# Optimization experiments

Measured on AMD Instinct MI355X. Metric: run time of the kernel, lower is better.

The kernel has to match this reference:

```python
import jax, jax.numpy as jnp
import numpy as np

NEG_INF = -1e30


def setup_inputs() -> dict:
    key = jax.random.key(0)
    k1, k2, k3, k4 = jax.random.split(key, 4)
    B, T, C, H = 4, 4096, 1024, 64
    x = jax.random.normal(k1, (B, T, C), dtype=jnp.float32)
    Wk = jax.random.normal(k2, (C, H), dtype=jnp.float32) * (C ** -0.5)
    Wq = jax.random.normal(k3, (C, H), dtype=jnp.float32) * (C ** -0.5)
    Wv = jax.random.normal(k4, (C, H), dtype=jnp.float32) * (C ** -0.5)
    return {"x": x, "Wk": Wk, "Wq": Wq, "Wv": Wv}


def reference(x, Wk, Wq, Wv):
    # x: [B, T, C]; Wq/Wk/Wv: [C, H]
    B, T, C = x.shape
    q = jnp.einsum('btc,ch->bth', x, Wq)  # [B,T,H]
    k = jnp.einsum('btc,ch->bth', x, Wk)  # [B,T,H]
    v = jnp.einsum('btc,ch->bth', x, Wv)  # [B,T,H]
    # NOTE: original scales by C**-0.5 (n_embd), not head_size**-0.5.
    scale = jnp.asarray(C, x.dtype) ** -0.5
    wei = jnp.einsum('bth,bsh->bts', q, k) * scale  # [B,T,T]
    causal = jnp.tril(jnp.ones((T, T), dtype=bool))
    wei = jnp.where(causal, wei, NEG_INF)
    wei = jax.nn.softmax(wei, axis=-1)
    # dropout p=0.0 -> identity
    out = jnp.einsum('bts,bsh->bth', wei, v)  # [B,T,H]
    return out
```

## Files before the change

kernel.cpp:

```cpp
#include <hip/hip_runtime.h>
#include <math.h>

typedef short bfx8 __attribute__((ext_vector_type(8)));
typedef short bfx4 __attribute__((ext_vector_type(4)));
typedef float fx4  __attribute__((ext_vector_type(4)));
typedef unsigned int ux2 __attribute__((ext_vector_type(2)));
typedef unsigned int ux4v __attribute__((ext_vector_type(4)));

__device__ __forceinline__ unsigned short f2bf(float f) {
    unsigned int u = __builtin_bit_cast(unsigned int, f);
    u += 0x7FFFu + ((u >> 16) & 1u);
    return (unsigned short)(u >> 16);
}
__device__ __forceinline__ float bf2f(unsigned short s) {
    unsigned int u = ((unsigned int)s) << 16;
    return __builtin_bit_cast(float, u);
}
__device__ __forceinline__ unsigned int cvtpk(float a, float b) {
    unsigned int d;
    asm("v_cvt_pk_bf16_f32 %0, %1, %2" : "=v"(d) : "v"(a), "v"(b));
    return d;
}

__global__ __launch_bounds__(256) void wt_prep(const float* __restrict__ Wq,
                                               const float* __restrict__ Wk,
                                               const float* __restrict__ Wv,
                                               unsigned short* __restrict__ wt)
{
    const int k0  = blockIdx.x * 64;
    const int mat = blockIdx.y;
    const float* W = (mat == 0) ? Wq : ((mat == 1) ? Wk : Wv);
    const float scale = (mat == 0) ? (0.03125f * 1.4426950408889634f) : 1.0f;
    __shared__ unsigned short Ls[64 * 68];
    const int t = threadIdx.x;
    #pragma unroll
    for (int i = 0; i < 4; ++i) {
        int idx4 = t + 256 * i;
        int r = idx4 >> 4, c4 = idx4 & 15;
        float4 v = *(const float4*)&W[(size_t)(k0 + r) * 64 + c4 * 4];
        Ls[r * 68 + c4 * 4 + 0] = f2bf(v.x * scale);
        Ls[r * 68 + c4 * 4 + 1] = f2bf(v.y * scale);
        Ls[r * 68 + c4 * 4 + 2] = f2bf(v.z * scale);
        Ls[r * 68 + c4 * 4 + 3] = f2bf(v.w * scale);
    }
    __syncthreads();
    #pragma unroll
    for (int i = 0; i < 2; ++i) {
        int u = t + 256 * i;
        int n = u >> 3, kc = u & 7;
        bfx8 o;
        #pragma unroll
        for (int j = 0; j < 8; ++j) o[j] = (short)Ls[(kc * 8 + j) * 68 + n];
        *(bfx8*)&wt[(size_t)(mat * 64 + n) * 1024 + k0 + kc * 8] = o;
    }
}

__global__ __launch_bounds__(256) void qkv_mfma(
    const float* __restrict__ x, const unsigned short* __restrict__ wt,
    unsigned short* __restrict__ qb, unsigned short* __restrict__ kb,
    unsigned short* __restrict__ vt)
{
    __shared__ alignas(16) char smem[57344];
    const int t = threadIdx.x;
    const int w = t >> 6, l = t & 63, g = l >> 4, li = l & 15;
    const int m0 = blockIdx.x * 32;
    const int rh  = (w & 1) * 16;
    const int nb0 = (w >> 1) * 6;

    fx4 acc[6];
    #pragma unroll
    for (int i = 0; i < 6; ++i) acc[i] = (fx4){0.f, 0.f, 0.f, 0.f};

    float4 xr[2];

    const unsigned short* wSrc[6];
    #pragma unroll
    for (int i = 0; i < 6; ++i) {
        int s = w * 6144 + i * 1024 + l * 16;
        int n = s >> 7, c = ((s >> 4) & 7) ^ (n & 7);
        wSrc[i] = wt + (size_t)n * 1024 + c * 8;
    }

#define QKV_DMA_W(K0, BI) do { \
    _Pragma("unroll") for (int i_ = 0; i_ < 6; ++i_) \
        __builtin_amdgcn_global_load_lds( \
            (const __attribute__((address_space(1))) void*)(wSrc[i_] + (K0)), \
            (__attribute__((address_space(3))) void*)(smem + 8192 + (BI) * 24576 + w * 6144 + i_ * 1024), \
            16, 0, 0); \
} while (0)

#define QKV_LOAD_X(K0) do { \
    _Pragma("unroll") for (int i_ = 0; i_ < 2; ++i_) { int idx4 = t + 256 * i_; int r_ = idx4 >> 4, c4 = idx4 & 15; \
        xr[i_] = *(const float4*)&x[(size_t)(m0 + r_) * 1024 + (K0) + c4 * 4]; } \
} while (0)

#define QKV_STORE_X(BI) do { \
    char* xb_ = smem + (BI) * 4096; \
    _Pragma("unroll") for (int i_ = 0; i_ < 2; ++i_) { int idx4 = t + 256 * i_; int r_ = idx4 >> 4, c4 = idx4 & 15; \
        ux2 u_; u_[0] = cvtpk(xr[i_].x, xr[i_].y); u_[1] = cvtpk(xr[i_].z, xr[i_].w); \
        *(ux2*)(xb_ + ((r_ * 128 + c4 * 8) ^ ((r_ & 7) << 4))) = u_; } \
} while (0)

    QKV_LOAD_X(0); QKV_STORE_X(0); QKV_DMA_W(0, 0);
    __syncthreads();

    for (int ch = 0; ch < 16; ++ch) {
        if (ch + 1 < 16) { QKV_DMA_W((ch + 1) * 64, (ch + 1) & 1); QKV_LOAD_X((ch + 1) * 64); }
        char* xb = smem + (ch & 1) * 4096;
        char* wb = smem + 8192 + (ch & 1) * 24576;
        const int arow = rh + li;
        #pragma unroll
        for (int kk = 0; kk < 2; ++kk) {
            bfx8 af = *(bfx8*)(xb + ((arow * 128 + kk * 64 + g * 16) ^ ((arow & 7) << 4)));
            #pragma unroll
            for (int nb = 0; nb < 6; ++nb) {
                int nrow = (nb0 + nb) * 16 + li;
                bfx8 bf = *(bfx8*)(wb + ((nrow * 128 + kk * 64 + g * 16) ^ ((nrow & 7) << 4)));
                acc[nb] = __builtin_amdgcn_mfma_f32_16x16x32_bf16(af, bf, acc[nb], 0, 0, 0);
            }
        }
        if (ch + 1 < 16) QKV_STORE_X((ch + 1) & 1);
        __syncthreads();
    }

    const int mrow = m0 + rh + g * 4;
    #pragma unroll
    for (int nb = 0; nb < 6; ++nb) {
        const int nbg = nb0 + nb;
        if (nbg < 4) {
            #pragma unroll
            for (int r = 0; r < 4; ++r)
                qb[(size_t)(mrow + r) * 64 + nbg * 16 + li] = f2bf(acc[nb][r]);
        } else if (nbg < 8) {
            #pragma unroll
            for (int r = 0; r < 4; ++r)
                kb[(size_t)(mrow + r) * 64 + (nbg - 4) * 16 + li] = f2bf(acc[nb][r]);
        }
    }

    __syncthreads();
    unsigned short* Vt = (unsigned short*)smem;
    #pragma unroll
    for (int nb = 0; nb < 6; ++nb) {
        const int nbg = nb0 + nb;
        if (nbg >= 8) {
            #pragma unroll
            for (int r = 0; r < 4; ++r)
                Vt[((nbg - 8) * 16 + li) * 40 + g * 8 + (rh >> 2) + r] = f2bf(acc[nb][r]);
        }
    }
    __syncthreads();
    const int bb = m0 >> 12, mt = m0 & 4095;
    {
        int d = t >> 2, c = t & 3;
        *(bfx8*)&vt[((size_t)(bb * 64 + d)) * 4096 + mt + c * 8] = *(bfx8*)&Vt[d * 40 + c * 8];
    }
}

__global__ __launch_bounds__(256, 4) void attn_mfma(
    const unsigned short* __restrict__ qb, const unsigned short* __restrict__ kb,
    const unsigned short* __restrict__ vt,
    unsigned short* __restrict__ pO, float* __restrict__ pml)
{
    __shared__ alignas(16) char smem[34816];
    const int t = threadIdx.x;
    const int w = t >> 6, l = t & 63, g = l >> 4, li = l & 15;
    const int bx = blockIdx.x;

    const int b = bx & 3;
    const int j = bx >> 2;
    int qt, seg, nch;
    if (j < 224) {
        int a = 1;
        #pragma unroll
        for (int aa = 2; aa <= 7; ++aa) if (j >= 4 * aa * (aa - 1)) a = aa;
        const int local = j - 4 * a * (a - 1);
        qt = 8 * a + local / a;
        seg = local % a;
        nch = 8;
    } else {
        const int jd = j - 224;
        const int r = 7 - (jd >> 3);
        const int a = jd & 7;
        qt = 8 * a + r; seg = a; nch = r + 1;
    }
    const int qbase = qt * 64;
    const int kvb = seg * 512;
    const int qsub = w & 1, par = w >> 1;
    const int qmax_w = qbase + qsub * 32 + 31;
    const int aq = qt >> 3, rq = qt & 7;
    const int slot = b * 288 + (aq + 1) * (4 * aq + rq) + seg;

    const unsigned short* Qg = qb + (size_t)b * 4096 * 64;
    const unsigned short* Kg = kb + (size_t)b * 4096 * 64;
    const unsigned short* Vg = vt + (size_t)b * 64 * 4096;

    const unsigned short* kSrc[2];
    const unsigned short* vSrc[2];
    #pragma unroll
    for (int i = 0; i < 2; ++i) {
        int s = w * 2048 + i * 1024 + l * 16;
        int r = s >> 7, c = ((s >> 4) & 7) ^ (r & 7);
        kSrc[i] = Kg + (size_t)r * 64 + c * 8;
        vSrc[i] = Vg + (size_t)r * 4096 + c * 8;
    }

#define ATT_DMA(CB, BI) do { \
    _Pragma("unroll") for (int i_ = 0; i_ < 2; ++i_) { \
        __builtin_amdgcn_global_load_lds( \
            (const __attribute__((address_space(1))) void*)(kSrc[i_] + (size_t)(CB) * 64), \
            (__attribute__((address_space(3))) void*)(smem + (BI) * 8192 + w * 2048 + i_ * 1024), 16, 0, 0); \
        __builtin_amdgcn_global_load_lds( \
            (const __attribute__((address_space(1))) void*)(vSrc[i_] + (CB)), \
            (__attribute__((address_space(3))) void*)(smem + 16384 + (BI) * 8192 + w * 2048 + i_ * 1024), 16, 0, 0); } \
} while (0)

    bfx8 qf[2][2];
    #pragma unroll
    for (int f = 0; f < 2; ++f)
        #pragma unroll
        for (int h = 0; h < 2; ++h)
            qf[f][h] = *(const bfx8*)&Qg[(size_t)(qbase + qsub * 32 + f * 16 + li) * 64 + h * 32 + g * 8];

    ATT_DMA(kvb, 0);
    __syncthreads();

    fx4 o[4][2];
    #pragma unroll
    for (int i = 0; i < 4; ++i)
        #pragma unroll
        for (int f = 0; f < 2; ++f) o[i][f] = (fx4){0.f, 0.f, 0.f, 0.f};
    float lsum[2] = {0.f, 0.f};

    for (int ch = 0; ch < nch; ++ch) {
        const int cb = kvb + (ch << 6);
        if (ch + 1 < nch) ATT_DMA(cb + 64, (ch + 1) & 1);
        char* ks = smem + (ch & 1) * 8192;
        char* vs = smem + 16384 + (ch & 1) * 8192;
        const int sub = cb + par * 32;
        if (sub <= qmax_w) {
            fx4 s[2][2];
            #pragma unroll
            for (int st = 0; st < 2; ++st)
                #pragma unroll
                for (int f = 0; f < 2; ++f) s[st][f] = (fx4){0.f, 0.f, 0.f, 0.f};
            __builtin_amdgcn_s_setprio(1);
            #pragma unroll
            for (int st = 0; st < 2; ++st) {
                const int krow = par * 32 + st * 16 + li;
                const int sw = (krow & 7) << 4;
                bfx8 kf0 = *(bfx8*)(ks + ((krow * 128 + g * 16) ^ sw));
                bfx8 kf1 = *(bfx8*)(ks + ((krow * 128 + 64 + g * 16) ^ sw));
                #pragma unroll
                for (int f = 0; f < 2; ++f) {
                    s[st][f] = __builtin_amdgcn_mfma_f32_16x16x32_bf16(kf0, qf[f][0], s[st][f], 0, 0, 0);
                    s[st][f] = __builtin_amdgcn_mfma_f32_16x16x32_bf16(kf1, qf[f][1], s[st][f], 0, 0, 0);
                }
            }
            __builtin_amdgcn_s_setprio(0);

            bfx8 pf[2];
            #pragma unroll
            for (int f = 0; f < 2; ++f) {
                const int qmin_f = qbase + qsub * 32 + f * 16;
                float p[8];
                if (sub + 31 > qmin_f) {
                    #pragma unroll
                    for (int st = 0; st < 2; ++st)
                        #pragma unroll
                        for (int rr = 0; rr < 4; ++rr) {
                            int kv = sub + st * 16 + 4 * g + rr;
                            p[st * 4 + rr] = (kv <= qmin_f + li) ? s[st][f][rr] : -1e30f;
                        }
                } else {
                    #pragma unroll
                    for (int st = 0; st < 2; ++st)
                        #pragma unroll
                        for (int rr = 0; rr < 4; ++rr) p[st * 4 + rr] = s[st][f][rr];
                }
                #pragma unroll
                for (int e = 0; e < 8; ++e) p[e] = exp2f(p[e]);
                lsum[f] += ((p[0]+p[1])+(p[2]+p[3])) + ((p[4]+p[5])+(p[6]+p[7]));
                ux4v pu;
                pu[0] = cvtpk(p[0], p[1]); pu[1] = cvtpk(p[2], p[3]);
                pu[2] = cvtpk(p[4], p[5]); pu[3] = cvtpk(p[6], p[7]);
                pf[f] = __builtin_bit_cast(bfx8, pu);
            }

            __builtin_amdgcn_s_setprio(1);
            #pragma unroll
            for (int dblk = 0; dblk < 4; ++dblk) {
                const int dr = dblk * 16 + li;
                bfx8 vf = *(bfx8*)(vs + ((dr * 128 + par * 64 + g * 16) ^ ((dr & 7) << 4)));
                #pragma unroll
                for (int f = 0; f < 2; ++f)
                    o[dblk][f] = __builtin_amdgcn_mfma_f32_16x16x32_bf16(vf, pf[f], o[dblk][f], 0, 0, 0);
            }
            __builtin_amdgcn_s_setprio(0);
        }
        __syncthreads();
    }

    float* Osh = (float*)smem;
    float* lsh = (float*)(smem + 32768);
    #pragma unroll
    for (int dblk = 0; dblk < 4; ++dblk)
        #pragma unroll
        for (int f = 0; f < 2; ++f)
            #pragma unroll
            for (int r = 0; r < 4; ++r)
                Osh[(par * 64 + qsub * 32 + f * 16 + li) * 64 + dblk * 16 + g * 4 + r] = o[dblk][f][r];
    #pragma unroll
    for (int f = 0; f < 2; ++f)
        lsh[((w * 2 + f) * 4 + g) * 16 + li] = lsum[f];
    __syncthreads();

    {
        const int q = t >> 2, dg = t & 3;
        const int A = (q >> 5), Bw = A + 2, fq = (q >> 4) & 1, liq = q & 15;
        float L = 0.f;
        #pragma unroll
        for (int gg2 = 0; gg2 < 4; ++gg2)
            L += lsh[((A * 2 + fq) * 4 + gg2) * 16 + liq] + lsh[((Bw * 2 + fq) * 4 + gg2) * 16 + liq];
        const float* OA = &Osh[q * 64 + dg * 16];
        const float* OB = &Osh[(64 + q) * 64 + dg * 16];
        ux4v u1, u2;
        u1[0] = cvtpk(OA[0] + OB[0],  OA[1] + OB[1]);
        u1[1] = cvtpk(OA[2] + OB[2],  OA[3] + OB[3]);
        u1[2] = cvtpk(OA[4] + OB[4],  OA[5] + OB[5]);
        u1[3] = cvtpk(OA[6] + OB[6],  OA[7] + OB[7]);
        u2[0] = cvtpk(OA[8] + OB[8],  OA[9] + OB[9]);
        u2[1] = cvtpk(OA[10] + OB[10], OA[11] + OB[11]);
        u2[2] = cvtpk(OA[12] + OB[12], OA[13] + OB[13]);
        u2[3] = cvtpk(OA[14] + OB[14], OA[15] + OB[15]);
        unsigned short* dst = pO + (size_t)slot * 4096 + q * 64 + dg * 16;
        *(bfx8*)&dst[0] = __builtin_bit_cast(bfx8, u1);
        *(bfx8*)&dst[8] = __builtin_bit_cast(bfx8, u2);
        if (dg == 0) pml[(size_t)slot * 64 + q] = L;
    }
}

__global__ __launch_bounds__(256) void attn_merge(
    const unsigned short* __restrict__ pO, const float* __restrict__ pml,
    float* __restrict__ out)
{
    const int b = blockIdx.x & 3, qt = blockIdx.x >> 2;
    const int a = qt >> 3, r = qt & 7;
    const int nseg = a + 1;
    const int slot0 = b * 288 + (a + 1) * (4 * a + r);
    const int t = threadIdx.x;
    const int q = t >> 2, dg = t & 3;

    float L = 0.f;
    float acc[16];
    #pragma unroll
    for (int jj = 0; jj < 16; ++jj) acc[jj] = 0.f;
    #pragma unroll
    for (int s = 0; s < 8; ++s) {
        if (s < nseg) {
            L += pml[(size_t)(slot0 + s) * 64 + q];
            const unsigned short* src = pO + (size_t)(slot0 + s) * 4096 + q * 64 + dg * 16;
            bfx8 v0 = *(const bfx8*)&src[0];
            bfx8 v1 = *(const bfx8*)&src[8];
            #pragma unroll
            for (int jj = 0; jj < 8; ++jj) acc[jj]     += bf2f((unsigned short)v0[jj]);
            #pragma unroll
            for (int jj = 0; jj < 8; ++jj) acc[8 + jj] += bf2f((unsigned short)v1[jj]);
        }
    }
    const float inv = 1.f / L;
    float* orow = out + ((size_t)b * 4096 + qt * 64 + q) * 64 + dg * 16;
    #pragma unroll
    for (int v4 = 0; v4 < 4; ++v4) {
        float4 rr;
        rr.x = acc[v4 * 4 + 0] * inv; rr.y = acc[v4 * 4 + 1] * inv;
        rr.z = acc[v4 * 4 + 2] * inv; rr.w = acc[v4 * 4 + 3] * inv;
        *(float4*)&orow[v4 * 4] = rr;
    }
}

extern "C" void kernel_launch(void* const* d_in, const int* in_sizes, int n_in,
                              void* d_out, int out_size, void* d_ws, size_t ws_size,
                              hipStream_t stream)
{
    const float* x  = (const float*)d_in[0];
    const float* Wk = (const float*)d_in[1];
    const float* Wq = (const float*)d_in[2];
    const float* Wv = (const float*)d_in[3];
    float* outp = (float*)d_out;

    char* ws = (char*)d_ws;
    unsigned short* qbuf = (unsigned short*)(ws);
    unsigned short* kbuf = (unsigned short*)(ws + 2*1024*1024);
    unsigned short* vtb  = (unsigned short*)(ws + 4*1024*1024);
    unsigned short* wtb  = (unsigned short*)(ws + 6*1024*1024);
    unsigned short* pO   = (unsigned short*)(ws + 7*1024*1024);
    float*          pml  = (float*)(ws + 16*1024*1024 + 512*1024);

    wt_prep<<<dim3(16, 3), 256, 0, stream>>>(Wq, Wk, Wv, wtb);
    qkv_mfma<<<512, 256, 0, stream>>>(x, wtb, qbuf, kbuf, vtb);
    attn_mfma<<<1152, 256, 0, stream>>>(qbuf, kbuf, vtb, pO, pml);
    attn_merge<<<256, 256, 0, stream>>>(pO, pml, outp);
}
```

Before: 56.55 us.

## Restructure attention into per-wave private KV pipelines with 32-row query tiles

Changes the attention split from 64-query tiles with 512-key segments to 32-query tiles with 1024-key segments. Each of the four waves now owns a strided quarter of the keys and keeps its own double-buffered K/V stream in LDS, synchronised only with vmcnt waits. This removes the per-chunk __syncthreads and lets waves run independently, and the workspace slot layout and merge kernel are rewritten to match. In exchange it uses 64KB of LDS, lowers occupancy to 2 blocks, and adds a 4-way reduction in the epilogue.

```diff
diff --git a/kernel.cpp b/kernel.cpp
--- a/kernel.cpp
+++ b/kernel.cpp
@@ -157,62 +157,69 @@
     }
 }
 
-__global__ __launch_bounds__(256, 4) void attn_mfma(
+__global__ __launch_bounds__(256, 2) void attn_mfma(
     const unsigned short* __restrict__ qb, const unsigned short* __restrict__ kb,
     const unsigned short* __restrict__ vt,
     unsigned short* __restrict__ pO, float* __restrict__ pml)
 {
-    __shared__ alignas(16) char smem[34816];
+    __shared__ alignas(16) char smem[65536];
     const int t = threadIdx.x;
     const int w = t >> 6, l = t & 63, g = l >> 4, li = l & 15;
     const int bx = blockIdx.x;
 
     const int b = bx & 3;
     const int j = bx >> 2;
-    int qt, seg, nch;
-    if (j < 224) {
-        int a = 1;
-        #pragma unroll
-        for (int aa = 2; aa <= 7; ++aa) if (j >= 4 * aa * (aa - 1)) a = aa;
-        const int local = j - 4 * a * (a - 1);
-        qt = 8 * a + local / a;
-        seg = local % a;
-        nch = 8;
+    int qt, seg;
+    if (j < 192) {
+        int a = (j >= 96) ? 3 : ((j >= 32) ? 2 : 1);
+        const int offs = 16 * a * (a - 1);
+        qt = 32 * a + (j - offs) / a;
+        seg = (j - offs) % a;
     } else {
-        const int jd = j - 224;
-        const int r = 7 - (jd >> 3);
-        const int a = jd & 7;
-        qt = 8 * a + r; seg = a; nch = r + 1;
-    }
-    const int qbase = qt * 64;
-    const int kvb = seg * 512;
-    const int qsub = w & 1, par = w >> 1;
-    const int qmax_w = qbase + qsub * 32 + 31;
-    const int aq = qt >> 3, rq = qt & 7;
-    const int slot = b * 288 + (aq + 1) * (4 * aq + rq) + seg;
+        const int jd = j - 192;
+        const int r = 31 - (jd >> 2);
+        const int a = jd & 3;
+        qt = 32 * a + r; seg = a;
+    }
+    const int qbase = qt * 32;
+    const int kvb = seg * 1024;
+    const int par = w;
+    const int aq = qt >> 5, rq = qt & 31;
+    const int slot = b * 320 + qt + 16 * aq * (aq - 1) + rq * aq + seg;
+
+    const int lastkv = qbase + 31 - 32 * par;
+    int nch = 0;
+    if (lastkv >= kvb) { nch = (lastkv - kvb) / 128 + 1; if (nch > 8) nch = 8; }
 
     const unsigned short* Qg = qb + (size_t)b * 4096 * 64;
     const unsigned short* Kg = kb + (size_t)b * 4096 * 64;
     const unsigned short* Vg = vt + (size_t)b * 64 * 4096;
 
-    const unsigned short* kSrc[2];
-    const unsigned short* vSrc[2];
-    #pragma unroll
-    for (int i = 0; i < 2; ++i) {
-        int s = w * 2048 + i * 1024 + l * 16;
-        int r = s >> 7, c = ((s >> 4) & 7) ^ (r & 7);
-        kSrc[i] = Kg + (size_t)r * 64 + c * 8;
-        vSrc[i] = Vg + (size_t)r * 4096 + c * 8;
-    }
-
-#define ATT_DMA(CB, BI) do { \
-    _Pragma("unroll") for (int i_ = 0; i_ < 2; ++i_) { \
+    char* const kB0 = smem + w * 16384;
+    char* const kB1 = kB0 + 4096;
+    char* const vB0 = kB0 + 8192;
+    char* const vB1 = kB0 + 12288;
+
+    const unsigned short* kSrc[4];
+    const unsigned short* vSrc[4];
+    #pragma unroll
+    for (int i = 0; i < 4; ++i) {
+        int ofs = i * 1024 + l * 16;
+        int row = ofs >> 7, sl = (ofs >> 4) & 7;
+        kSrc[i] = Kg + (size_t)row * 64 + (sl ^ (row & 7)) * 8;
+        int u = sl ^ (row & 7);
+        int d = row + 32 * (u >> 2), gq = u & 3;
+        vSrc[i] = Vg + (size_t)d * 4096 + gq * 8;
+    }
+
+#define ATT_DMA(KVS, KB, VB) do { \
+    _Pragma("unroll") for (int i_ = 0; i_ < 4; ++i_) { \
         __builtin_amdgcn_global_load_lds( \
-            (const __attribute__((address_space(1))) void*)(kSrc[i_] + (size_t)(CB) * 64), \
-            (__attribute__((address_space(3))) void*)(smem + (BI) * 8192 + w * 2048 + i_ * 1024), 16, 0, 0); \
+            (const __attribute__((address_space(1))) void*)(kSrc[i_] + (size_t)(KVS) * 64), \
+            (__attribute__((address_space(3))) void*)((KB) + i_ * 1024), 16, 0, 0); \
         __builtin_amdgcn_global_load_lds( \
-            (const __attribute__((address_space(1))) void*)(vSrc[i_] + (CB)), \
-            (__attribute__((address_space(3))) void*)(smem + 16384 + (BI) * 8192 + w * 2048 + i_ * 1024), 16, 0, 0); } \
+            (const __attribute__((address_space(1))) void*)(vSrc[i_] + (KVS)), \
+            (__attribute__((address_space(3))) void*)((VB) + i_ * 1024), 16, 0, 0); } \
 } while (0)
 
     bfx8 qf[2][2];
@@ -220,10 +227,7 @@
     for (int f = 0; f < 2; ++f)
         #pragma unroll
         for (int h = 0; h < 2; ++h)
-            qf[f][h] = *(const bfx8*)&Qg[(size_t)(qbase + qsub * 32 + f * 16 + li) * 64 + h * 32 + g * 8];
-
-    ATT_DMA(kvb, 0);
-    __syncthreads();
+            qf[f][h] = *(const bfx8*)&Qg[(size_t)(qbase + f * 16 + li) * 64 + h * 32 + g * 8];
 
     fx4 o[4][2];
     #pragma unroll
@@ -232,13 +236,18 @@
         for (int f = 0; f < 2; ++f) o[i][f] = (fx4){0.f, 0.f, 0.f, 0.f};
     float lsum[2] = {0.f, 0.f};
 
-    for (int ch = 0; ch < nch; ++ch) {
-        const int cb = kvb + (ch << 6);
-        if (ch + 1 < nch) ATT_DMA(cb + 64, (ch + 1) & 1);
-        char* ks = smem + (ch & 1) * 8192;
-        char* vs = smem + 16384 + (ch & 1) * 8192;
-        const int sub = cb + par * 32;
-        if (sub <= qmax_w) {
+    if (nch > 0) {
+        ATT_DMA(kvb + par * 32, kB0, vB0);
+        if (nch > 1) ATT_DMA(kvb + 128 + par * 32, kB1, vB1);
+
+        for (int ch = 0; ch < nch; ++ch) {
+            const int kvs = kvb + (ch << 7) + par * 32;
+            if (ch < nch - 1) { asm volatile("s_waitcnt vmcnt(8)" ::: "memory"); }
+            else              { asm volatile("s_waitcnt vmcnt(0)" ::: "memory"); }
+            __builtin_amdgcn_sched_barrier(0);
+            char* ks = (ch & 1) ? kB1 : kB0;
+            char* vs = (ch & 1) ? vB1 : vB0;
+
             fx4 s[2][2];
             #pragma unroll
             for (int st = 0; st < 2; ++st)
@@ -247,10 +256,10 @@
             __builtin_amdgcn_s_setprio(1);
             #pragma unroll
             for (int st = 0; st < 2; ++st) {
-                const int krow = par * 32 + st * 16 + li;
+                const int krow = st * 16 + li;
                 const int sw = (krow & 7) << 4;
-                bfx8 kf0 = *(bfx8*)(ks + ((krow * 128 + g * 16) ^ sw));
-                bfx8 kf1 = *(bfx8*)(ks + ((krow * 128 + 64 + g * 16) ^ sw));
+                bfx8 kf0 = *(bfx8*)(ks + (krow * 128 + (g * 16 ^ sw)));
+                bfx8 kf1 = *(bfx8*)(ks + (krow * 128 + ((64 + g * 16) ^ sw)));
                 #pragma unroll
                 for (int f = 0; f < 2; ++f) {
                     s[st][f] = __builtin_amdgcn_mfma_f32_16x16x32_bf16(kf0, qf[f][0], s[st][f], 0, 0, 0);
@@ -262,14 +271,14 @@
             bfx8 pf[2];
             #pragma unroll
             for (int f = 0; f < 2; ++f) {
-                const int qmin_f = qbase + qsub * 32 + f * 16;
+                const int qmin_f = qbase + f * 16;
                 float p[8];
-                if (sub + 31 > qmin_f) {
+                if (kvs + 31 > qmin_f) {
                     #pragma unroll
                     for (int st = 0; st < 2; ++st)
                         #pragma unroll
                         for (int rr = 0; rr < 4; ++rr) {
-                            int kv = sub + st * 16 + 4 * g + rr;
+                            int kv = kvs + st * 16 + 4 * g + rr;
                             p[st * 4 + rr] = (kv <= qmin_f + li) ? s[st][f][rr] : -1e30f;
                         }
                 } else {
@@ -291,16 +300,23 @@
             #pragma unroll
             for (int dblk = 0; dblk < 4; ++dblk) {
                 const int dr = dblk * 16 + li;
-                bfx8 vf = *(bfx8*)(vs + ((dr * 128 + par * 64 + g * 16) ^ ((dr & 7) << 4)));
+                const int s8 = ((dr >> 5) * 4 + g) ^ (dr & 7);
+                bfx8 vf = *(bfx8*)(vs + (dr & 31) * 128 + s8 * 16);
                 #pragma unroll
                 for (int f = 0; f < 2; ++f)
                     o[dblk][f] = __builtin_amdgcn_mfma_f32_16x16x32_bf16(vf, pf[f], o[dblk][f], 0, 0, 0);
             }
             __builtin_amdgcn_s_setprio(0);
-        }
-        __syncthreads();
-    }
-
+
+            if (ch + 2 < nch) {
+                asm volatile("s_waitcnt lgkmcnt(0)" ::: "memory");
+                __builtin_amdgcn_sched_barrier(0);
+                ATT_DMA(kvs + 256, ks, vs);
+            }
+        }
+    }
+
+    __syncthreads();
     float* Osh = (float*)smem;
     float* lsh = (float*)(smem + 32768);
     #pragma unroll
@@ -309,34 +325,35 @@
         for (int f = 0; f < 2; ++f)
             #pragma unroll
             for (int r = 0; r < 4; ++r)
-                Osh[(par * 64 + qsub * 32 + f * 16 + li) * 64 + dblk * 16 + g * 4 + r] = o[dblk][f][r];
+                Osh[(par * 32 + f * 16 + li) * 64 + dblk * 16 + g * 4 + r] = o[dblk][f][r];
     #pragma unroll
     for (int f = 0; f < 2; ++f)
-        lsh[((w * 2 + f) * 4 + g) * 16 + li] = lsum[f];
+        lsh[((par * 2 + f) * 4 + g) * 16 + li] = lsum[f];
     __syncthreads();
 
     {
-        const int q = t >> 2, dg = t & 3;
-        const int A = (q >> 5), Bw = A + 2, fq = (q >> 4) & 1, liq = q & 15;
+        const int q = t >> 3, dgi = t & 7;
+        const int fq = q >> 4, liq = q & 15;
         float L = 0.f;
         #pragma unroll
-        for (int gg2 = 0; gg2 < 4; ++gg2)
-            L += lsh[((A * 2 + fq) * 4 + gg2) * 16 + liq] + lsh[((Bw * 2 + fq) * 4 + gg2) * 16 + liq];
-        const float* OA = &Osh[q * 64 + dg * 16];
-        const float* OB = &Osh[(64 + q) * 64 + dg * 16];
-        ux4v u1, u2;
-        u1[0] = cvtpk(OA[0] + OB[0],  OA[1] + OB[1]);
-        u1[1] = cvtpk(OA[2] + OB[2],  OA[3] + OB[3]);
-        u1[2] = cvtpk(OA[4] + OB[4],  OA[5] + OB[5]);
-        u1[3] = cvtpk(OA[6] + OB[6],  OA[7] + OB[7]);
-        u2[0] = cvtpk(OA[8] + OB[8],  OA[9] + OB[9]);
-        u2[1] = cvtpk(OA[10] + OB[10], OA[11] + OB[11]);
-        u2[2] = cvtpk(OA[12] + OB[12], OA[13] + OB[13]);
-        u2[3] = cvtpk(OA[14] + OB[14], OA[15] + OB[15]);
-        unsigned short* dst = pO + (size_t)slot * 4096 + q * 64 + dg * 16;
-        *(bfx8*)&dst[0] = __builtin_bit_cast(bfx8, u1);
-        *(bfx8*)&dst[8] = __builtin_bit_cast(bfx8, u2);
-        if (dg == 0) pml[(size_t)slot * 64 + q] = L;
+        for (int pp = 0; pp < 4; ++pp)
+            #pragma unroll
+            for (int gg = 0; gg < 4; ++gg)
+                L += lsh[((pp * 2 + fq) * 4 + gg) * 16 + liq];
+        float a8[8];
+        #pragma unroll
+        for (int jj = 0; jj < 8; ++jj) a8[jj] = 0.f;
+        #pragma unroll
+        for (int pp = 0; pp < 4; ++pp) {
+            const float* src = &Osh[(pp * 32 + q) * 64 + dgi * 8];
+            #pragma unroll
+            for (int jj = 0; jj < 8; ++jj) a8[jj] += src[jj];
+        }
+        ux4v u1;
+        u1[0] = cvtpk(a8[0], a8[1]); u1[1] = cvtpk(a8[2], a8[3]);
+        u1[2] = cvtpk(a8[4], a8[5]); u1[3] = cvtpk(a8[6], a8[7]);
+        *(bfx8*)&pO[(size_t)slot * 2048 + q * 64 + dgi * 8] = __builtin_bit_cast(bfx8, u1);
+        if (dgi == 0) pml[(size_t)slot * 32 + q] = L;
     }
 }
 
@@ -345,38 +362,32 @@
     float* __restrict__ out)
 {
     const int b = blockIdx.x & 3, qt = blockIdx.x >> 2;
-    const int a = qt >> 3, r = qt & 7;
+    const int a = qt >> 5, r = qt & 31;
     const int nseg = a + 1;
-    const int slot0 = b * 288 + (a + 1) * (4 * a + r);
+    const int slot0 = b * 320 + qt + 16 * a * (a - 1) + r * a;
     const int t = threadIdx.x;
-    const int q = t >> 2, dg = t & 3;
+    const int q = t >> 3, dgi = t & 7;
 
     float L = 0.f;
-    float acc[16];
-    #pragma unroll
-    for (int jj = 0; jj < 16; ++jj) acc[jj] = 0.f;
-    #pragma unroll
-    for (int s = 0; s < 8; ++s) {
+    float acc[8];
+    #pragma unroll
+    for (int jj = 0; jj < 8; ++jj) acc[jj] = 0.f;
+    #pragma unroll
+    for (int s = 0; s < 4; ++s) {
         if (s < nseg) {
-            L += pml[(size_t)(slot0 + s) * 64 + q];
-            const unsigned short* src = pO + (size_t)(slot0 + s) * 4096 + q * 64 + dg * 16;
-            bfx8 v0 = *(const bfx8*)&src[0];
-            bfx8 v1 = *(const bfx8*)&src[8];
-            #pragma unroll
-            for (int jj = 0; jj < 8; ++jj) acc[jj]     += bf2f((unsigned short)v0[jj]);
-            #pragma unroll
-            for (int jj = 0; jj < 8; ++jj) acc[8 + jj] += bf2f((unsigned short)v1[jj]);
+            L += pml[(size_t)(slot0 + s) * 32 + q];
+            bfx8 v = *(const bfx8*)&pO[(size_t)(slot0 + s) * 2048 + q * 64 + dgi * 8];
+            #pragma unroll
+            for (int jj = 0; jj < 8; ++jj) acc[jj] += bf2f((unsigned short)v[jj]);
         }
     }
     const float inv = 1.f / L;
-    float* orow = out + ((size_t)b * 4096 + qt * 64 + q) * 64 + dg * 16;
-    #pragma unroll
-    for (int v4 = 0; v4 < 4; ++v4) {
-        float4 rr;
-        rr.x = acc[v4 * 4 + 0] * inv; rr.y = acc[v4 * 4 + 1] * inv;
-        rr.z = acc[v4 * 4 + 2] * inv; rr.w = acc[v4 * 4 + 3] * inv;
-        *(float4*)&orow[v4 * 4] = rr;
-    }
+    float* orow = out + ((size_t)b * 4096 + qt * 32 + q) * 64 + dgi * 8;
+    float4 r0, r1;
+    r0.x = acc[0] * inv; r0.y = acc[1] * inv; r0.z = acc[2] * inv; r0.w = acc[3] * inv;
+    r1.x = acc[4] * inv; r1.y = acc[5] * inv; r1.z = acc[6] * inv; r1.w = acc[7] * inv;
+    *(float4*)&orow[0] = r0;
+    *(float4*)&orow[4] = r1;
 }
 
 extern "C" void kernel_launch(void* const* d_in, const int* in_sizes, int n_in,
@@ -395,10 +406,10 @@
     unsigned short* vtb  = (unsigned short*)(ws + 4*1024*1024);
     unsigned short* wtb  = (unsigned short*)(ws + 6*1024*1024);
     unsigned short* pO   = (unsigned short*)(ws + 7*1024*1024);
-    float*          pml  = (float*)(ws + 16*1024*1024 + 512*1024);
+    float*          pml  = (float*)(ws + 13*1024*1024);
 
     wt_prep<<<dim3(16, 3), 256, 0, stream>>>(Wq, Wk, Wv, wtb);
     qkv_mfma<<<512, 256, 0, stream>>>(x, wtb, qbuf, kbuf, vtb);
-    attn_mfma<<<1152, 256, 0, stream>>>(qbuf, kbuf, vtb, pO, pml);
-    attn_merge<<<256, 256, 0, stream>>>(pO, pml, outp);
-}
+    attn_mfma<<<1280, 256, 0, stream>>>(qbuf, kbuf, vtb, pO, pml);
+    attn_merge<<<512, 256, 0, stream>>>(pO, pml, outp);
+}
```

New measurement: 58.71 us. 3.8% more time.
